# Kernel optimization log

Hardware: AMD Instinct MI355X
Metric: run time of the kernel (lower is better)

The kernel has to match this reference:

```python
import jax, jax.numpy as jnp
import numpy as np

IN_DIM = 128
LAYER_DIMS = [128, 128]
NUM_SAMPLES = [25, 10]
L0 = 3072
NEG_WEIGHT = 1.0


def setup_inputs() -> dict:
    key = jax.random.key(0)
    ks = jax.random.split(key, 12)
    feat = jax.random.normal(ks[0], (L0, IN_DIM), dtype=jnp.float32)
    nodes = jax.random.randint(ks[1], (L0,), 0, L0)
    nb0 = jnp.arange(L0)
    nb1 = jax.random.randint(ks[2], (L0 * 10,), 0, L0)
    nb2 = jax.random.randint(ks[3], (L0 * 10 * 25,), 0, L0)
    src_idx = jax.random.randint(ks[4], (1024,), 0, L0)
    pos_idx = jax.random.randint(ks[5], (1024,), 0, L0)
    neg_idx = jax.random.randint(ks[6], (512,), 0, L0)
    g = 0.05
    # mean aggregator weights: layer0 in=IN_DIM, layer1 in=2*128 (concat)
    w_self_0 = jax.random.normal(ks[7], (IN_DIM, 128), jnp.float32) * g
    w_neigh_0 = jax.random.normal(ks[8], (IN_DIM, 128), jnp.float32) * g
    w_self_1 = jax.random.normal(ks[9], (256, 128), jnp.float32) * g
    w_neigh_1 = jax.random.normal(ks[10], (256, 128), jnp.float32) * g
    return dict(nodes=nodes, feat=feat, src_idx=src_idx, pos_idx=pos_idx,
                neg_idx=neg_idx, nb0=nb0, nb1=nb1, nb2=nb2,
                w_self_0=w_self_0, w_neigh_0=w_neigh_0,
                w_self_1=w_self_1, w_neigh_1=w_neigh_1)


def _aggregate(hidden, params):
    # GraphSAGE layer stack: at layer l, combine each hop with the mean of its
    # sampled neighbors, concat self/neigh transforms, relu except last layer.
    num_layers = len(NUM_SAMPLES)
    for layer in range(num_layers):
        w_self, w_neigh = params[layer]
        is_last = layer == num_layers - 1
        next_hidden = []
        for hop in range(num_layers - layer):
            s = NUM_SAMPLES[num_layers - hop - 1]
            self_v = hidden[hop]  # [n, d]
            neigh = hidden[hop + 1].reshape(self_v.shape[0], s, self_v.shape[1])
            neigh_mean = jnp.mean(neigh, axis=1)
            h = jnp.concatenate([self_v @ w_self, neigh_mean @ w_neigh], axis=1)
            if not is_last:
                h = jax.nn.relu(h)
            next_hidden.append(h)
        hidden = next_hidden
    return hidden[0]


def _l2_normalize(x, eps=1e-12):
    return x * jax.lax.rsqrt(jnp.maximum(jnp.sum(x * x, axis=1, keepdims=True), eps))


def reference(nodes, feat, src_idx, pos_idx, neg_idx, nb0, nb1, nb2,
              w_self_0, w_neigh_0, w_self_1, w_neigh_1):
    hidden = [feat[nb0], feat[nb1], feat[nb2]]
    params = [(w_self_0, w_neigh_0), (w_self_1, w_neigh_1)]
    output = _aggregate(hidden, params)          # [L0, 256]
    output = _l2_normalize(output)
    src_emb = output[src_idx]                    # [B, 256]
    pos_emb = output[pos_idx]
    neg_emb = output[neg_idx]                    # [Nneg, 256]

    aff = jnp.sum(src_emb * pos_emb, axis=1)     # [B]
    neg_aff = src_emb @ neg_emb.T                # [B, Nneg]

    # MRR via double argsort (tf double top_k equivalent; ties -> positive last)
    aff_all = jnp.concatenate([neg_aff, aff[:, None]], axis=1)
    order = jnp.argsort(-aff_all, axis=1, stable=True)
    ranks = jnp.argsort(order, axis=1, stable=True)
    mrr = jnp.mean(1.0 / (ranks[:, -1].astype(jnp.float32) + 1.0))

    # sigmoid cross-entropy: labels 1 -> softplus(-x); labels 0 -> softplus(x)
    true_xent = jax.nn.softplus(-aff)
    neg_xent = jax.nn.softplus(neg_aff)
    loss = jnp.sum(true_xent) + NEG_WEIGHT * jnp.sum(neg_xent)
    loss = loss / jnp.asarray(src_emb.shape[0], jnp.float32)
    return src_emb, loss, mrr
```

## Files before the change

### kernel.cpp

```cpp
#include <hip/hip_runtime.h>
#include <math.h>

#define L0      3072
#define BATCH   1024
#define NNEG    512


__device__ __forceinline__ float bf2f(unsigned short u) {
  return __uint_as_float(((unsigned)u) << 16);
}
__device__ __forceinline__ void store_out(float v, float* p) { *p = v; }
__device__ __forceinline__ void store_out(float v, unsigned short* p) {
  unsigned x = __float_as_uint(v);
  *p = (unsigned short)((x + 0x7fff + ((x >> 16) & 1)) >> 16);
}

template<int K, int AW, int HOFF, bool NORM, typename OutT>
__global__ __launch_bounds__(512) void k_mm(
    const float* __restrict__ Ain,
    const float* __restrict__ W0, const float* __restrict__ W1,
    OutT* __restrict__ Out, const int ldo, const int outHalfOff,
    float* __restrict__ zbuf, const int zcount) {
  __shared__ float AT[6 * AW];
  __shared__ float rs[8][3];
  const int t = threadIdx.x;
  if (zbuf != nullptr && blockIdx.x == 0)
    for (int z = t; z < zcount; z += 512) zbuf[z] = 0.f;
  const int base = blockIdx.x * 6;
  {
    const float4* __restrict__ src = (const float4*)(Ain + base * AW);
    float4* __restrict__ dst = (float4*)AT;
    for (int idx = t; idx < 6 * AW / 4; idx += 512) dst[idx] = src[idx];
  }
  __syncthreads();

  const int wave = t >> 6;
  const int half = wave >> 2;
  const int colg = (wave >> 1) & 1;
  const int rowg = wave & 1;
  const int rg = rowg * 3;
  const int col = colg * 64 + (t & 63);
  const float* __restrict__ W = (half ? W1 : W0) + col;
  const float* __restrict__ A0 = AT + rg * AW + half * HOFF;

  float acc[3] = {0.f, 0.f, 0.f};
#pragma unroll 4
  for (int d = 0; d < K; d += 4) {
    float4 a[3];
#pragma unroll
    for (int r = 0; r < 3; ++r) a[r] = *(const float4*)&A0[r * AW + d];
    float w[4];
#pragma unroll
    for (int i2 = 0; i2 < 4; ++i2) w[i2] = W[(d + i2) * 128];
#pragma unroll
    for (int i2 = 0; i2 < 4; ++i2)
#pragma unroll
      for (int r = 0; r < 3; ++r)
        acc[r] = fmaf(((const float*)&a[r])[i2], w[i2], acc[r]);
  }

  float scale[3] = {1.f, 1.f, 1.f};
  if (NORM) {
    float p[3];
#pragma unroll
    for (int r = 0; r < 3; ++r) p[r] = acc[r] * acc[r];
#pragma unroll
    for (int off = 32; off > 0; off >>= 1)
#pragma unroll
      for (int r = 0; r < 3; ++r) p[r] += __shfl_xor(p[r], off, 64);
    if ((t & 63) == 0) { rs[wave][0] = p[0]; rs[wave][1] = p[1]; rs[wave][2] = p[2]; }
    __syncthreads();
#pragma unroll
    for (int r = 0; r < 3; ++r) {
      const float s = rs[rowg][r] + rs[rowg + 2][r] + rs[rowg + 4][r] + rs[rowg + 6][r];
      scale[r] = rsqrtf(fmaxf(s, 1e-12f));
    }
  }
  OutT* __restrict__ O = Out + half * outHalfOff;
#pragma unroll
  for (int r = 0; r < 3; ++r)
    store_out(acc[r] * scale[r], &O[(base + rg + r) * ldo + col]);
}

__global__ __launch_bounds__(640) void k_aggregate(
    const unsigned short* __restrict__ X0, const unsigned short* __restrict__ Y0,
    const int* __restrict__ nb0, const int* __restrict__ nb1,
    const int* __restrict__ nb2, float* __restrict__ H) {
  __shared__ float gB[10][128], gC[10][128], gD[10][128];
  const int i = blockIdx.x;
  const int t = threadIdx.x;
  const int n0 = nb0[i];
  const int j = t >> 6;
  const int lam = t & 63;
  const int r = i * 10 + j;
  int myidx = 0;
  if (lam < 25) myidx = nb2[r * 25 + lam];
  else if (lam == 25) myidx = nb1[r];
  const int c8 = lam & 15;
  const int sub = lam >> 4;

  float d8[8];
#pragma unroll
  for (int e = 0; e < 8; ++e) d8[e] = 0.f;
#pragma unroll
  for (int m = 0; m < 7; ++m) {
    const int k = sub + 4 * m;
    const int ridx = __shfl(myidx, k, 64);
    if (k < 25) {
      const float4 raw = *(const float4*)(Y0 + ridx * 128 + c8 * 8);
      const unsigned short* u = (const unsigned short*)&raw;
#pragma unroll
      for (int e = 0; e < 8; ++e) d8[e] += bf2f(u[e]);
    }
  }
#pragma unroll
  for (int e = 0; e < 8; ++e) d8[e] += __shfl_xor(d8[e], 16, 64);
#pragma unroll
  for (int e = 0; e < 8; ++e) d8[e] += __shfl_xor(d8[e], 32, 64);

  const int r1 = __shfl(myidx, 25, 64);
  if (sub == 0) {
#pragma unroll
    for (int e = 0; e < 8; ++e) gD[j][c8 * 8 + e] = fmaxf(d8[e] * 0.04f, 0.f);
    const float4 raw = *(const float4*)(Y0 + r1 * 128 + c8 * 8);
    const unsigned short* u = (const unsigned short*)&raw;
#pragma unroll
    for (int e = 0; e < 8; ++e) gB[j][c8 * 8 + e] = bf2f(u[e]);
  } else if (sub == 1) {
    const float4 raw = *(const float4*)(X0 + r1 * 128 + c8 * 8);
    const unsigned short* u = (const unsigned short*)&raw;
#pragma unroll
    for (int e = 0; e < 8; ++e) gC[j][c8 * 8 + e] = fmaxf(bf2f(u[e]), 0.f);
  }
  __syncthreads();

  if (t < 512) {
    const int q = t >> 7, c = t & 127;
    float v;
    if (q == 0) {
      v = fmaxf(bf2f(X0[n0 * 128 + c]), 0.f);
    } else {
      const float* g = (q == 1) ? &gB[0][0] : (q == 2) ? &gC[0][0] : &gD[0][0];
      float s = 0.f;
#pragma unroll
      for (int jj = 0; jj < 10; ++jj) s += g[jj * 128 + c];
      v = s * 0.1f;
      if (q == 1) v = fmaxf(v, 0.f);
    }
    H[i * 512 + t] = v;
  }
}

__device__ __forceinline__ float softplusf(float x) {
  return fmaxf(x, 0.f) + log1pf(expf(-fabsf(x)));
}

__global__ __launch_bounds__(256) void k_neg(
    const float* __restrict__ O, const int* __restrict__ src_idx,
    const int* __restrict__ pos_idx, const int* __restrict__ neg_idx,
    float* __restrict__ out_src, int* __restrict__ rank,
    float* __restrict__ spPos, float* __restrict__ spNeg) {
  __shared__ float SL[32][129];
  __shared__ float NL[64][129];
  __shared__ float affL[32];
  __shared__ int cntL[32];
  const int t = threadIdx.x;
  const int rowBase = (blockIdx.x >> 3) * 32;
  const int colBase = (blockIdx.x & 7) * 64;
  const bool first = (colBase == 0);
  if (t < 32) {
    const int b = rowBase + t;
    const float* __restrict__ ps = O + src_idx[b] * 256;
    const float* __restrict__ pp = O + pos_idx[b] * 256;
    float a = 0.f;
#pragma unroll 16
    for (int d = 0; d < 256; ++d) a = fmaf(ps[d], pp[d], a);
    affL[t] = a;
    cntL[t] = 0;
    if (first) atomicAdd(spPos, softplusf(-a));
  }
  if (first) {
    for (int idx = t; idx < 32 * 64; idx += 256) {
      const int rr = idx >> 6, qq = idx & 63;
      ((float4*)out_src)[(rowBase + rr) * 64 + qq] =
          ((const float4*)O)[src_idx[rowBase + rr] * 64 + qq];
    }
  }
  const int ct = t & 31;
  const int rt = t >> 5;
  float acc[4][2];
#pragma unroll
  for (int k = 0; k < 4; ++k) { acc[k][0] = 0.f; acc[k][1] = 0.f; }
  for (int ch = 0; ch < 2; ++ch) {
    __syncthreads();
    for (int idx = t; idx < 32 * 128; idx += 256) {
      int r = idx >> 7, dd = idx & 127;
      SL[r][dd] = O[src_idx[rowBase + r] * 256 + ch * 128 + dd];
    }
    for (int idx = t; idx < 64 * 128; idx += 256) {
      int cpos = idx >> 7, dd = idx & 127;
      NL[cpos][dd] = O[neg_idx[colBase + cpos] * 256 + ch * 128 + dd];
    }
    __syncthreads();
    for (int dd = 0; dd < 128; ++dd) {
      float n0 = NL[ct][dd], n1 = NL[ct + 32][dd];
#pragma unroll
      for (int k = 0; k < 4; ++k) {
        float sv = SL[rt + 8 * k][dd];
        acc[k][0] = fmaf(sv, n0, acc[k][0]);
        acc[k][1] = fmaf(sv, n1, acc[k][1]);
      }
    }
  }
  float sp = 0.f;
#pragma unroll
  for (int k = 0; k < 4; ++k) {
    float a = affL[rt + 8 * k];
    int cnt = 0;
#pragma unroll
    for (int cc = 0; cc < 2; ++cc) {
      float v = acc[k][cc];
      sp += softplusf(v);
      cnt += (v >= a) ? 1 : 0;
    }
    if (cnt) atomicAdd(&cntL[rt + 8 * k], cnt);
  }
#pragma unroll
  for (int off = 32; off > 0; off >>= 1) sp += __shfl_down(sp, off, 64);
  if ((t & 63) == 0) atomicAdd(spNeg, sp);
  __syncthreads();
  if (t < 32) atomicAdd(&rank[rowBase + t], cntL[t]);
}

__global__ __launch_bounds__(256) void k_finalize(
    const int* __restrict__ rank, const float* __restrict__ spPos,
    const float* __restrict__ spNeg, float* __restrict__ out) {
  const int t = threadIdx.x;
  float s = 0.f;
  for (int i = t; i < BATCH; i += 256) s += 1.f / (float)(rank[i] + 1);
#pragma unroll
  for (int off = 32; off > 0; off >>= 1) s += __shfl_down(s, off, 64);
  __shared__ float wsum[4];
  if ((t & 63) == 0) wsum[t >> 6] = s;
  __syncthreads();
  if (t == 0) {
    float mrr = (wsum[0] + wsum[1] + wsum[2] + wsum[3]) * (1.f / 1024.f);
    float loss = (spPos[0] + spNeg[0]) * (1.f / 1024.f);
    out[BATCH * 256]     = loss;
    out[BATCH * 256 + 1] = mrr;
  }
}

extern "C" void kernel_launch(void* const* d_in, const int* in_sizes, int n_in,
                              void* d_out, int out_size, void* d_ws, size_t ws_size,
                              hipStream_t stream) {
  const float* feat   = (const float*)d_in[1];
  const int* src_idx  = (const int*)d_in[2];
  const int* pos_idx  = (const int*)d_in[3];
  const int* neg_idx  = (const int*)d_in[4];
  const int* nb0      = (const int*)d_in[5];
  const int* nb1      = (const int*)d_in[6];
  const int* nb2      = (const int*)d_in[7];
  const float* ws0    = (const float*)d_in[8];
  const float* wn0    = (const float*)d_in[9];
  const float* ws1    = (const float*)d_in[10];
  const float* wn1    = (const float*)d_in[11];

  float* wsf = (float*)d_ws;
  unsigned short* X0 = (unsigned short*)d_ws;
  unsigned short* Y0 = X0 + 393216;
  float* H     = wsf + 393216;
  float* R     = wsf + 1966080;
  float* spPos = wsf + 2752512;
  float* spNeg = wsf + 2752513;
  int*   rank  = (int*)(wsf + 2752514);
  float* out   = (float*)d_out;

  k_mm<128, 128, 0, false, unsigned short><<<L0 / 6, 512, 0, stream>>>(
      feat, ws0, wn0, X0, 128, 393216, spPos, 1026);
  k_aggregate<<<L0, 640, 0, stream>>>(X0, Y0, nb0, nb1, nb2, H);
  k_mm<256, 512, 256, true, float><<<L0 / 6, 512, 0, stream>>>(
      H, ws1, wn1, R, 256, 128, nullptr, 0);
  k_neg<<<(BATCH / 32) * (NNEG / 64), 256, 0, stream>>>(
      R, src_idx, pos_idx, neg_idx, out, rank, spPos, spNeg);
  k_finalize<<<1, 256, 0, stream>>>(rank, spPos, spNeg, out);
}
```

Measured before the change: 166.7 us.

## Retile negative-affinity kernel and fold finalize into last-block reduction

The negative-affinity kernel is retiled to 16 rows by 128 negatives per 128-thread block. It uses a single padded LDS buffer loaded with float4 gathers, and each thread computes a 4x4 register tile. The positive affinity is now computed from LDS in the same loop rather than by separate strided global loads. The separate finalize launch is removed: a done counter (zeroed with the other accumulators) elects the last block to compute MRR and loss, saving one kernel launch at the cost of a threadfence and atomic ticket per block. The grid shrinks from 256 blocks of 256 threads to 256 blocks of 128 threads, which reduces parallelism.

Measured after the change: 165.2 us. Within noise of the previous version (-0.9%).

```diff
diff --git a/kernel.cpp b/kernel.cpp
--- a/kernel.cpp
+++ b/kernel.cpp
@@ -155,99 +155,134 @@
   return fmaxf(x, 0.f) + log1pf(expf(-fabsf(x)));
 }
 
-__global__ __launch_bounds__(256) void k_neg(
+__global__ __launch_bounds__(128) void k_neg(
     const float* __restrict__ O, const int* __restrict__ src_idx,
     const int* __restrict__ pos_idx, const int* __restrict__ neg_idx,
     float* __restrict__ out_src, int* __restrict__ rank,
-    float* __restrict__ spPos, float* __restrict__ spNeg) {
-  __shared__ float SL[32][129];
-  __shared__ float NL[64][129];
-  __shared__ float affL[32];
-  __shared__ int cntL[32];
+    float* __restrict__ spPos, float* __restrict__ spNeg,
+    int* __restrict__ done) {
+  __shared__ float lds[160 * 132];
+  __shared__ int rowIdx[160];
+  __shared__ float affL[16];
+  __shared__ int cntL[16];
+  __shared__ float wsum[2];
+  __shared__ int lastDone;
   const int t = threadIdx.x;
-  const int rowBase = (blockIdx.x >> 3) * 32;
-  const int colBase = (blockIdx.x & 7) * 64;
+  const int rowBase = (blockIdx.x >> 2) * 16;
+  const int colBase = (blockIdx.x & 3) * 128;
   const bool first = (colBase == 0);
-  if (t < 32) {
-    const int b = rowBase + t;
-    const float* __restrict__ ps = O + src_idx[b] * 256;
-    const float* __restrict__ pp = O + pos_idx[b] * 256;
-    float a = 0.f;
-#pragma unroll 16
-    for (int d = 0; d < 256; ++d) a = fmaf(ps[d], pp[d], a);
-    affL[t] = a;
-    cntL[t] = 0;
-    if (first) atomicAdd(spPos, softplusf(-a));
-  }
+
+  if (t < 16) { cntL[t] = 0; rowIdx[t] = src_idx[rowBase + t]; }
+  else if (t < 32) rowIdx[t] = pos_idx[rowBase + t - 16];
+  if (t >= 32) rowIdx[t] = neg_idx[colBase + t - 32];
+  if (t < 32) rowIdx[128 + t] = neg_idx[colBase + 96 + t];
+
   if (first) {
-    for (int idx = t; idx < 32 * 64; idx += 256) {
-      const int rr = idx >> 6, qq = idx & 63;
-      ((float4*)out_src)[(rowBase + rr) * 64 + qq] =
-          ((const float4*)O)[src_idx[rowBase + rr] * 64 + qq];
-    }
-  }
-  const int ct = t & 31;
-  const int rt = t >> 5;
-  float acc[4][2];
-#pragma unroll
-  for (int k = 0; k < 4; ++k) { acc[k][0] = 0.f; acc[k][1] = 0.f; }
+    const float4* __restrict__ s4 = (const float4*)O;
+    float4* __restrict__ d4o = (float4*)out_src;
+#pragma unroll
+    for (int idx = t; idx < 16 * 64; idx += 128) {
+      const int rr = idx >> 6, c4 = idx & 63;
+      d4o[(rowBase + rr) * 64 + c4] = s4[src_idx[rowBase + rr] * 64 + c4];
+    }
+  }
+  __syncthreads();
+
+  const int tc = t & 31;
+  const int tr = t >> 5;
+  float acc[4][4];
+#pragma unroll
+  for (int k = 0; k < 4; ++k)
+#pragma unroll
+    for (int j = 0; j < 4; ++j) acc[k][j] = 0.f;
+  float aff = 0.f;
+
   for (int ch = 0; ch < 2; ++ch) {
+    if (ch) __syncthreads();
+    {
+      const float4* __restrict__ s4 = (const float4*)O;
+#pragma unroll 4
+      for (int idx = t; idx < 160 * 32; idx += 128) {
+        const int row = idx >> 5, c4 = idx & 31;
+        *(float4*)&lds[row * 132 + c4 * 4] = s4[rowIdx[row] * 64 + ch * 32 + c4];
+      }
+    }
     __syncthreads();
-    for (int idx = t; idx < 32 * 128; idx += 256) {
-      int r = idx >> 7, dd = idx & 127;
-      SL[r][dd] = O[src_idx[rowBase + r] * 256 + ch * 128 + dd];
-    }
-    for (int idx = t; idx < 64 * 128; idx += 256) {
-      int cpos = idx >> 7, dd = idx & 127;
-      NL[cpos][dd] = O[neg_idx[colBase + cpos] * 256 + ch * 128 + dd];
-    }
+#pragma unroll 2
+    for (int d4 = 0; d4 < 32; ++d4) {
+      float4 a[4], b[4];
+#pragma unroll
+      for (int k = 0; k < 4; ++k)
+        a[k] = *(const float4*)&lds[(tr + 4 * k) * 132 + d4 * 4];
+#pragma unroll
+      for (int j = 0; j < 4; ++j)
+        b[j] = *(const float4*)&lds[(32 + tc + 32 * j) * 132 + d4 * 4];
+      float4 sv, pv;
+      if (t < 16) {
+        sv = *(const float4*)&lds[t * 132 + d4 * 4];
+        pv = *(const float4*)&lds[(16 + t) * 132 + d4 * 4];
+      }
+#pragma unroll
+      for (int i2 = 0; i2 < 4; ++i2) {
+#pragma unroll
+        for (int k = 0; k < 4; ++k)
+#pragma unroll
+          for (int j = 0; j < 4; ++j)
+            acc[k][j] = fmaf(((const float*)&a[k])[i2],
+                             ((const float*)&b[j])[i2], acc[k][j]);
+        if (t < 16)
+          aff = fmaf(((const float*)&sv)[i2], ((const float*)&pv)[i2], aff);
+      }
+    }
+  }
+  if (t < 16) affL[t] = aff;
+  __syncthreads();
+
+  float sp = 0.f;
+#pragma unroll
+  for (int k = 0; k < 4; ++k) {
+    const float av = affL[tr + 4 * k];
+    int cnt = 0;
+#pragma unroll
+    for (int j = 0; j < 4; ++j) {
+      const float v = acc[k][j];
+      sp += softplusf(v);
+      cnt += (v >= av) ? 1 : 0;
+    }
+    if (cnt) atomicAdd(&cntL[tr + 4 * k], cnt);
+  }
+#pragma unroll
+  for (int off = 32; off > 0; off >>= 1) sp += __shfl_down(sp, off, 64);
+  if ((t & 63) == 0) wsum[t >> 6] = sp;
+  if (first && t < 16) atomicAdd(spPos, softplusf(-aff));
+  __syncthreads();
+  if (t == 0) atomicAdd(spNeg, wsum[0] + wsum[1]);
+  if (t < 16) atomicAdd(&rank[rowBase + t], cntL[t]);
+
+  __threadfence();
+  __syncthreads();
+  if (t == 0) lastDone = (atomicAdd(done, 1) == 255) ? 1 : 0;
+  __syncthreads();
+  if (lastDone) {
+    float s = 0.f;
+    for (int i = t; i < BATCH; i += 128) {
+      const int rv = __hip_atomic_load(&rank[i], __ATOMIC_RELAXED,
+                                       __HIP_MEMORY_SCOPE_AGENT);
+      s += 1.f / (float)(rv + 1);
+    }
+#pragma unroll
+    for (int off = 32; off > 0; off >>= 1) s += __shfl_down(s, off, 64);
+    if ((t & 63) == 0) wsum[t >> 6] = s;
     __syncthreads();
-    for (int dd = 0; dd < 128; ++dd) {
-      float n0 = NL[ct][dd], n1 = NL[ct + 32][dd];
-#pragma unroll
-      for (int k = 0; k < 4; ++k) {
-        float sv = SL[rt + 8 * k][dd];
-        acc[k][0] = fmaf(sv, n0, acc[k][0]);
-        acc[k][1] = fmaf(sv, n1, acc[k][1]);
-      }
-    }
-  }
-  float sp = 0.f;
-#pragma unroll
-  for (int k = 0; k < 4; ++k) {
-    float a = affL[rt + 8 * k];
-    int cnt = 0;
-#pragma unroll
-    for (int cc = 0; cc < 2; ++cc) {
-      float v = acc[k][cc];
-      sp += softplusf(v);
-      cnt += (v >= a) ? 1 : 0;
-    }
-    if (cnt) atomicAdd(&cntL[rt + 8 * k], cnt);
-  }
-#pragma unroll
-  for (int off = 32; off > 0; off >>= 1) sp += __shfl_down(sp, off, 64);
-  if ((t & 63) == 0) atomicAdd(spNeg, sp);
-  __syncthreads();
-  if (t < 32) atomicAdd(&rank[rowBase + t], cntL[t]);
-}
-
-__global__ __launch_bounds__(256) void k_finalize(
-    const int* __restrict__ rank, const float* __restrict__ spPos,
-    const float* __restrict__ spNeg, float* __restrict__ out) {
-  const int t = threadIdx.x;
-  float s = 0.f;
-  for (int i = t; i < BATCH; i += 256) s += 1.f / (float)(rank[i] + 1);
-#pragma unroll
-  for (int off = 32; off > 0; off >>= 1) s += __shfl_down(s, off, 64);
-  __shared__ float wsum[4];
-  if ((t & 63) == 0) wsum[t >> 6] = s;
-  __syncthreads();
-  if (t == 0) {
-    float mrr = (wsum[0] + wsum[1] + wsum[2] + wsum[3]) * (1.f / 1024.f);
-    float loss = (spPos[0] + spNeg[0]) * (1.f / 1024.f);
-    out[BATCH * 256]     = loss;
-    out[BATCH * 256 + 1] = mrr;
+    if (t == 0) {
+      const float mrr = (wsum[0] + wsum[1]) * (1.f / 1024.f);
+      const float p = __hip_atomic_load(spPos, __ATOMIC_RELAXED,
+                                        __HIP_MEMORY_SCOPE_AGENT);
+      const float n = __hip_atomic_load(spNeg, __ATOMIC_RELAXED,
+                                        __HIP_MEMORY_SCOPE_AGENT);
+      out_src[BATCH * 256]     = (p + n) * (1.f / 1024.f);
+      out_src[BATCH * 256 + 1] = mrr;
+    }
   }
 }
 
@@ -274,14 +309,14 @@
   float* spPos = wsf + 2752512;
   float* spNeg = wsf + 2752513;
   int*   rank  = (int*)(wsf + 2752514);
+  int*   done  = rank + 1024;
   float* out   = (float*)d_out;
 
   k_mm<128, 128, 0, false, unsigned short><<<L0 / 6, 512, 0, stream>>>(
-      feat, ws0, wn0, X0, 128, 393216, spPos, 1026);
+      feat, ws0, wn0, X0, 128, 393216, spPos, 1027);
   k_aggregate<<<L0, 640, 0, stream>>>(X0, Y0, nb0, nb1, nb2, H);
   k_mm<256, 512, 256, true, float><<<L0 / 6, 512, 0, stream>>>(
       H, ws1, wn1, R, 256, 128, nullptr, 0);
-  k_neg<<<(BATCH / 32) * (NNEG / 64), 256, 0, stream>>>(
-      R, src_idx, pos_idx, neg_idx, out, rank, spPos, spNeg);
-  k_finalize<<<1, 256, 0, stream>>>(rank, spPos, spNeg, out);
-}
+  k_neg<<<256, 128, 0, stream>>>(
+      R, src_idx, pos_idx, neg_idx, out, rank, spPos, spNeg, done);
+}
```
